# Kernel optimization log

Hardware: AMD Instinct MI355X
Metric: run time of the kernel (lower is better)

Reference implementation:

```python
import jax, jax.numpy as jnp
import numpy as np

V = 32000   # vocab
T = 256     # context len
C = 384     # n_embed
H = 6       # heads
D = 64      # head dim (HEAD_SIZE // NUM_HEADS)
L = 6       # blocks
B = 16      # batch
FF = 4 * C


def setup_inputs() -> dict:
    key = jax.random.key(0)
    ks = jax.random.split(key, 16)
    s = 0.02
    p = {}
    p["x_ids"] = jax.random.randint(ks[0], (B, T), 0, V)
    p["y_ids"] = jax.random.randint(ks[1], (B, T), 0, V)
    p["tok_emb"] = jax.random.normal(ks[2], (V, C), jnp.float32) * s
    p["pos_emb"] = jax.random.normal(ks[3], (T, C), jnp.float32) * s
    p["Wq"] = jax.random.normal(ks[4], (L, H, C, D), jnp.float32) * s
    p["Wk"] = jax.random.normal(ks[5], (L, H, C, D), jnp.float32) * s
    p["Wv"] = jax.random.normal(ks[6], (L, H, C, D), jnp.float32) * s
    p["Wo"] = jax.random.normal(ks[7], (L, H * D, C), jnp.float32) * s
    p["bo"] = jnp.zeros((L, C), jnp.float32)
    p["ln1_s"] = jnp.ones((L, C), jnp.float32)
    p["ln1_b"] = jnp.zeros((L, C), jnp.float32)
    p["ln2_s"] = jnp.ones((L, C), jnp.float32)
    p["ln2_b"] = jnp.zeros((L, C), jnp.float32)
    p["W1"] = jax.random.normal(ks[8], (L, C, FF), jnp.float32) * s
    p["b1"] = jnp.zeros((L, FF), jnp.float32)
    p["W2"] = jax.random.normal(ks[9], (L, FF, C), jnp.float32) * s
    p["b2"] = jnp.zeros((L, C), jnp.float32)
    p["lnf_s"] = jnp.ones((C,), jnp.float32)
    p["lnf_b"] = jnp.zeros((C,), jnp.float32)
    p["Whead"] = jax.random.normal(ks[10], (C, V), jnp.float32) * s
    p["bhead"] = jnp.zeros((V,), jnp.float32)
    return p


def _ln(x, scale, bias, eps=1e-5):
    m = x.mean(-1, keepdims=True)
    v = ((x - m) ** 2).mean(-1, keepdims=True)
    return (x - m) * jax.lax.rsqrt(v + eps) * scale + bias


def reference(x_ids, y_ids, tok_emb, pos_emb, Wq, Wk, Wv, Wo, bo,
              ln1_s, ln1_b, ln2_s, ln2_b, W1, b1, W2, b2,
              lnf_s, lnf_b, Whead, bhead):
    Bq, Tq = x_ids.shape
    x = tok_emb[x_ids] + pos_emb[:Tq]                      # [B,T,C]
    mask = jnp.tril(jnp.ones((Tq, Tq), bool))
    scale = C ** -0.5  # NOTE: original scales by input dim C, not head dim
    for l in range(L):
        h = _ln(x, ln1_s[l], ln1_b[l])
        q = jnp.einsum('btc,hcd->bhtd', h, Wq[l])
        k = jnp.einsum('btc,hcd->bhtd', h, Wk[l])
        v = jnp.einsum('btc,hcd->bhtd', h, Wv[l])
        att = jnp.einsum('bhtd,bhsd->bhts', q, k) * scale
        att = jnp.where(mask, att, -jnp.inf)
        att = jax.nn.softmax(att, axis=-1)
        o = jnp.einsum('bhts,bhsd->bhtd', att, v)
        o = o.transpose(0, 2, 1, 3).reshape(Bq, Tq, H * D)  # concat heads
        x = x + o @ Wo[l] + bo[l]
        h2 = _ln(x, ln2_s[l], ln2_b[l])
        x = x + jax.nn.relu(h2 @ W1[l] + b1[l]) @ W2[l] + b2[l]
    x = _ln(x, lnf_s, lnf_b)
    logits = x @ Whead + bhead                             # [B,T,V]
    logp = jax.nn.log_softmax(logits, axis=-1)
    loss = -jnp.take_along_axis(logp, y_ids[..., None], axis=-1).mean()
    return (logits, loss)
```

## Files before the change

### kernel.cpp

```cpp
#include <hip/hip_runtime.h>

typedef unsigned short u16;
typedef u16   u16x8 __attribute__((ext_vector_type(8)));
typedef short s16x8 __attribute__((ext_vector_type(8)));
typedef float f32x4 __attribute__((ext_vector_type(4)));

#define NV 32000
#define NT 256
#define NC 384
#define NH 6
#define ND 64
#define NL 6
#define NB 16
#define NFF 1536
#define NM (NB*NT)
#define QKVSZ (NB*NH*NT*ND)
#define NSLAB (NV/64)

__device__ __forceinline__ u16 f2bf(float f){
    unsigned x = __builtin_bit_cast(unsigned, f);
    x += 0x7fffu + ((x>>16)&1u);
    return (u16)(x>>16);
}

__device__ __forceinline__ void gload_lds16(const u16* g, u16* l){
    __builtin_amdgcn_global_load_lds((const __attribute__((address_space(1))) unsigned int*)g,
                                     (__attribute__((address_space(3))) unsigned int*)l, 16, 0, 0);
}

template<int N> __device__ __forceinline__ void wait_vm(){
    static_assert(N>=0 && N<=4, "add literal");
    if constexpr (N==0) asm volatile("s_waitcnt vmcnt(0)" ::: "memory");
    if constexpr (N==4) asm volatile("s_waitcnt vmcnt(4)" ::: "memory");
}
__device__ __forceinline__ void bar(){
    asm volatile("" ::: "memory");
    __builtin_amdgcn_s_barrier();
    asm volatile("" ::: "memory");
}

__global__ __launch_bounds__(256) void embed_ln(const int* __restrict__ ids,
        const float* __restrict__ tok, const float* __restrict__ pos,
        const float* __restrict__ sc, const float* __restrict__ bi,
        float* __restrict__ x, u16* __restrict__ out){
    int row  = blockIdx.x*4 + (threadIdx.x>>6);
    int lane = threadIdx.x & 63;
    int t = row & (NT-1);
    const float* tr = tok + (size_t)ids[row]*NC;
    const float* pr = pos + (size_t)t*NC;
    float* xr = x + (size_t)row*NC;
    float v[6]; float sum = 0.f, sq = 0.f;
    #pragma unroll
    for (int i=0;i<6;++i){
        int c = lane+64*i;
        v[i] = tr[c] + pr[c];
        xr[c] = v[i];
        sum += v[i]; sq += v[i]*v[i];
    }
    #pragma unroll
    for (int off=1; off<64; off<<=1){ sum += __shfl_xor(sum,off); sq += __shfl_xor(sq,off); }
    float mean = sum*(1.f/NC);
    float rstd = rsqrtf(sq*(1.f/NC) - mean*mean + 1e-5f);
    u16* orow = out + (size_t)row*NC;
    #pragma unroll
    for (int i=0;i<6;++i){ int c = lane+64*i; orow[c] = f2bf((v[i]-mean)*rstd*sc[c] + bi[c]); }
}

__global__ __launch_bounds__(256) void ln_kernel(const float* __restrict__ x,
        const float* __restrict__ sc, const float* __restrict__ bi, u16* __restrict__ out){
    int row  = blockIdx.x*4 + (threadIdx.x>>6);
    int lane = threadIdx.x & 63;
    const float* xr = x + (size_t)row*NC;
    float v[6]; float sum = 0.f, sq = 0.f;
    #pragma unroll
    for (int i=0;i<6;++i){ v[i]=xr[lane+64*i]; sum+=v[i]; sq+=v[i]*v[i]; }
    #pragma unroll
    for (int off=1; off<64; off<<=1){ sum += __shfl_xor(sum,off); sq += __shfl_xor(sq,off); }
    float mean = sum*(1.f/NC);
    float rstd = rsqrtf(sq*(1.f/NC) - mean*mean + 1e-5f);
    u16* orow = out + (size_t)row*NC;
    #pragma unroll
    for (int i=0;i<6;++i){ int c = lane+64*i; orow[c] = f2bf((v[i]-mean)*rstd*sc[c] + bi[c]); }
}

struct TDesc {
    const float* in; u16* out;
    int Cc; int nx; int perZ; int obDiv; int oStride; int start;
    long inBatch; long oS1; long oS2; float scale;
};
struct TPack { TDesc d[7]; };

__global__ __launch_bounds__(256) void tconv_all(TPack p){
    __shared__ float tile[32][33];
    int bid = blockIdx.x;
    int e = 0;
    #pragma unroll
    for (int i=1;i<7;++i) e += (bid >= p.d[i].start) ? 1 : 0;
    TDesc D = p.d[e];
    int local = bid - D.start;
    int bz  = local / D.perZ; int rem = local - bz*D.perZ;
    int cy  = rem / D.nx;     int cx  = rem - cy*D.nx;
    int r0 = cy*32, c0 = cx*32;
    const float* ib = D.in + (size_t)bz*D.inBatch;
    u16* ob = D.out + (size_t)(bz/D.obDiv)*D.oS1 + (size_t)(bz%D.obDiv)*D.oS2;
    int tx = threadIdx.x & 31, ty = threadIdx.x >> 5;
    #pragma unroll
    for (int i=0;i<4;++i) tile[ty+8*i][tx] = ib[(size_t)(r0+ty+8*i)*D.Cc + (c0+tx)];
    __syncthreads();
    #pragma unroll
    for (int i=0;i<4;++i) ob[(size_t)(c0+ty+8*i)*D.oStride + (r0+tx)] = f2bf(tile[tx][ty+8*i]*D.scale);
}

template<int EPI, int BM, int BN>
__global__ __launch_bounds__(256,4) void gemm_bt(
        const u16* __restrict__ A, const u16* __restrict__ Bt,
        const float* __restrict__ bias, float* __restrict__ resid,
        u16* __restrict__ outb,
        int M, int N, int K){
    constexpr int WM = BM/2, WN = BN/2, MI = WM/16, NI = WN/16;
    __shared__ u16 As[2*BM*32];
    __shared__ u16 Bs[2*BN*32];
    int tid = threadIdx.x;
    int lane = tid & 63, wid = tid >> 6;
    int wm = wid >> 1, wn = wid & 1;
    int l15 = lane & 15, lg = lane >> 4;
    int bx = blockIdx.x, by = blockIdx.y;
    int m0 = by * BM, n0 = bx * BN;
    f32x4 acc[MI][NI];
    #pragma unroll
    for (int a=0;a<MI;++a)
        #pragma unroll
        for (int b=0;b<NI;++b) acc[a][b] = f32x4{0.f,0.f,0.f,0.f};

    int nk = K >> 6;
    for (int kk = 0; kk < nk; ++kk){
        int k0 = kk << 6;
        #pragma unroll
        for (int h=0;h<2;++h){
            if constexpr (BM >= 64){
                #pragma unroll
                for (int i=0;i<BM/64;++i){
                    int o   = i*4096 + tid*16;
                    int row = o >> 6;
                    int kb  = (o & 63) >> 1;
                    gload_lds16(A + (size_t)(m0+row)*K + (k0+h*32+kb), &As[h*BM*32 + (o>>1)]);
                }
            } else {
                if (tid < BM*4){
                    int o = tid*16;
                    int row = o >> 6;
                    int kb  = (o & 63) >> 1;
                    gload_lds16(A + (size_t)(m0+row)*K + (k0+h*32+kb), &As[h*BM*32 + (o>>1)]);
                }
            }
            #pragma unroll
            for (int i=0;i<BN/64;++i){
                int o   = i*4096 + tid*16;
                int row = o >> 6;
                int kb  = (o & 63) >> 1;
                gload_lds16(Bt + (size_t)(n0+row)*K + (k0+h*32+kb), &Bs[h*BN*32 + (o>>1)]);
            }
        }
        asm volatile("s_waitcnt vmcnt(0)" ::: "memory");
        __syncthreads();
        #pragma unroll
        for (int ks=0;ks<2;++ks){
            s16x8 af[MI];
            #pragma unroll
            for (int mi=0;mi<MI;++mi) af[mi] = *(const s16x8*)&As[ks*BM*32 + (wm*WM+mi*16+l15)*32 + lg*8];
            #pragma unroll
            for (int ni=0;ni<NI;++ni){
                s16x8 bfr = *(const s16x8*)&Bs[ks*BN*32 + (wn*WN+ni*16+l15)*32 + lg*8];
                #pragma unroll
                for (int mi=0;mi<MI;++mi)
                    acc[mi][ni] = __builtin_amdgcn_mfma_f32_16x16x32_bf16(af[mi], bfr, acc[mi][ni], 0,0,0);
            }
        }
        __syncthreads();
    }

    #pragma unroll
    for (int mi=0;mi<MI;++mi){
        #pragma unroll
        for (int ni=0;ni<NI;++ni){
            #pragma unroll
            for (int r=0;r<4;++r){
                int mg = m0 + wm*WM + mi*16 + lg*4 + r;
                int ng = n0 + wn*WN + ni*16 + l15;
                float c = acc[mi][ni][r];
                if (EPI == 0){
                    int which = ng / NC; int hd = ng - which*NC;
                    int hh = hd >> 6, d = hd & 63;
                    int bb = mg >> 8, tt = mg & (NT-1);
                    outb[(size_t)which*QKVSZ + ((size_t)(bb*NH+hh)*NT + tt)*ND + d] = f2bf(c);
                } else if (EPI == 1){
                    float* pp = resid + (size_t)mg*N + ng;
                    *pp = *pp + c + bias[ng];
                } else if (EPI == 2){
                    outb[(size_t)mg*N + ng] = f2bf(fmaxf(c + bias[ng], 0.f));
                }
            }
        }
    }
}

__global__ __launch_bounds__(256,4) void gemm_head(
        const u16* __restrict__ A, const u16* __restrict__ Bt,
        const float* __restrict__ bias,
        float* __restrict__ outf, float* __restrict__ lpart,
        int M, int N, int K){
    constexpr int BM=128, BN=128, WM=64, WN=64, MI=4, NI=4;
    __shared__ u16 As[2][BM*32];
    __shared__ u16 Bs[2][BN*32];
    int tid = threadIdx.x;
    int lane = tid & 63, wid = tid >> 6;
    int wm = wid >> 1, wn = wid & 1;
    int l15 = lane & 15, lg = lane >> 4;
    int nwg = gridDim.x*gridDim.y;
    int orig = blockIdx.y*gridDim.x + blockIdx.x;
    int swz = (orig&7)*(nwg>>3) + (orig>>3);
    int by = swz & 31;
    int bx = swz >> 5;
    int m0 = by * BM, n0 = bx * BN;
    f32x4 acc[MI][NI];
    #pragma unroll
    for (int a=0;a<MI;++a)
        #pragma unroll
        for (int b=0;b<NI;++b) acc[a][b] = f32x4{0.f,0.f,0.f,0.f};

    auto STAGE = [&](int kt, int buf){
        int k0 = kt << 5;
        #pragma unroll
        for (int i=0;i<2;++i){
            int o   = i*4096 + tid*16;
            int row = o >> 6;
            int kb  = (o & 63) >> 1;
            gload_lds16(A + (size_t)(m0+row)*K + (k0+kb), &As[buf][o>>1]);
        }
        #pragma unroll
        for (int i=0;i<2;++i){
            int o   = i*4096 + tid*16;
            int row = o >> 6;
            int kb  = (o & 63) >> 1;
            gload_lds16(Bt + (size_t)(n0+row)*K + (k0+kb), &Bs[buf][o>>1]);
        }
    };

    int nk = K >> 5;
    STAGE(0, 0);
    for (int t = 0; t < nk; ++t){
        int buf = t & 1;
        if (t+1 < nk){ STAGE(t+1, buf^1); wait_vm<4>(); }
        else         { wait_vm<0>(); }
        bar();
        s16x8 af[MI];
        #pragma unroll
        for (int mi=0;mi<MI;++mi) af[mi] = *(const s16x8*)&As[buf][(wm*WM+mi*16+l15)*32 + lg*8];
        #pragma unroll
        for (int ni=0;ni<NI;++ni){
            s16x8 bfr = *(const s16x8*)&Bs[buf][(wn*WN+ni*16+l15)*32 + lg*8];
            #pragma unroll
            for (int mi=0;mi<MI;++mi)
                acc[mi][ni] = __builtin_amdgcn_mfma_f32_16x16x32_bf16(af[mi], bfr, acc[mi][ni], 0,0,0);
        }
        bar();
    }

    float es[MI][4];
    #pragma unroll
    for (int mi=0;mi<MI;++mi)
        #pragma unroll
        for (int r=0;r<4;++r) es[mi][r] = 0.f;
    #pragma unroll
    for (int mi=0;mi<MI;++mi)
        #pragma unroll
        for (int ni=0;ni<NI;++ni)
            #pragma unroll
            for (int r=0;r<4;++r){
                int mg = m0 + wm*WM + mi*16 + lg*4 + r;
                int ng = n0 + wn*WN + ni*16 + l15;
                float val = acc[mi][ni][r] + bias[ng];
                outf[(size_t)mg*N + ng] = val;
                es[mi][r] += __expf(val);
            }
    #pragma unroll
    for (int mi=0;mi<MI;++mi)
        #pragma unroll
        for (int r=0;r<4;++r){
            float s = es[mi][r];
            s += __shfl_xor(s,1); s += __shfl_xor(s,2);
            s += __shfl_xor(s,4); s += __shfl_xor(s,8);
            if (l15 == 0){
                int mg = m0 + wm*WM + mi*16 + lg*4 + r;
                lpart[(size_t)mg*NSLAB + bx*2 + wn] = s;
            }
        }
}

__global__ __launch_bounds__(256,2) void attn_kernel(const u16* __restrict__ qkv, u16* __restrict__ o){
    int blk = blockIdx.x;
    int qt = blk & 3, bh = blk >> 2;
    int b = bh / NH, h = bh - b*NH;
    int tid = threadIdx.x, lane = tid & 63, w = tid >> 6;
    int l15 = lane & 15, lg = lane >> 4;
    __shared__ u16 Ks[256*72];
    __shared__ u16 Vt[64*264];
    __shared__ u16 Ps[4][16*72];
    const u16* qb = qkv + (size_t)bh*NT*ND;
    const u16* kb = qb + QKVSZ;
    const u16* vb = kb + QKVSZ;
    int nit = (qt+1)*2;
    for (int it=0; it<nit; ++it){
        int idx = it*256 + tid;
        int e0 = idx*8;
        int row = e0 >> 6, col = e0 & 63;
        *(u16x8*)&Ks[row*72+col] = *(const u16x8*)(kb + e0);
        u16x8 vv = *(const u16x8*)(vb + e0);
        #pragma unroll
        for (int j=0;j<8;++j) Vt[(col+j)*264 + row] = vv[j];
    }
    const u16* qrow = qb + (size_t)(qt*64 + w*16 + l15)*ND;
    s16x8 qf[2];
    qf[0] = *(const s16x8*)(qrow + lg*8);
    qf[1] = *(const s16x8*)(qrow + 32 + lg*8);
    __syncthreads();

    f32x4 oacc[4]; float l_[4];
    #pragma unroll
    for (int c=0;c<4;++c){ oacc[c]=f32x4{0.f,0.f,0.f,0.f}; l_[c]=0.f; }
    u16* Pw = &Ps[w][0];

    for (int kt=0; kt<=qt; ++kt){
        f32x4 sacc[4];
        #pragma unroll
        for (int c=0;c<4;++c) sacc[c]=f32x4{0.f,0.f,0.f,0.f};
        #pragma unroll
        for (int ks=0;ks<2;++ks){
            s16x8 kf[4];
            #pragma unroll
            for (int ni=0;ni<4;++ni)
                kf[ni] = *(const s16x8*)&Ks[(kt*64+ni*16+l15)*72 + ks*32 + lg*8];
            #pragma unroll
            for (int ni=0;ni<4;++ni)
                sacc[ni] = __builtin_amdgcn_mfma_f32_16x16x32_bf16(qf[ks], kf[ni], sacc[ni], 0,0,0);
        }
        if (kt == qt){
            #pragma unroll
            for (int ni=0;ni<4;++ni)
                #pragma unroll
                for (int r=0;r<4;++r)
                    if (ni*16+l15 > w*16+lg*4+r) sacc[ni][r] = -1e30f;
        }
        #pragma unroll
        for (int r=0;r<4;++r){
            float rs = 0.f;
            #pragma unroll
            for (int ni=0;ni<4;++ni){
                float p = __expf(sacc[ni][r]);
                sacc[ni][r] = p;
                rs += p;
                Pw[(lg*4+r)*72 + ni*16 + l15] = f2bf(p);
            }
            rs += __shfl_xor(rs,1); rs += __shfl_xor(rs,2);
            rs += __shfl_xor(rs,4); rs += __shfl_xor(rs,8);
            l_[r] += rs;
        }
        #pragma unroll
        for (int ks=0;ks<2;++ks){
            s16x8 pf, vf[4];
            pf = *(const s16x8*)&Pw[l15*72 + ks*32 + lg*8];
            #pragma unroll
            for (int ni=0;ni<4;++ni)
                vf[ni] = *(const s16x8*)&Vt[(ni*16+l15)*264 + kt*64 + ks*32 + lg*8];
            #pragma unroll
            for (int ni=0;ni<4;++ni)
                oacc[ni] = __builtin_amdgcn_mfma_f32_16x16x32_bf16(pf, vf[ni], oacc[ni], 0,0,0);
        }
    }
    #pragma unroll
    for (int ni=0;ni<4;++ni)
        #pragma unroll
        for (int r=0;r<4;++r){
            int t = qt*64 + w*16 + lg*4 + r;
            int d = ni*16 + l15;
            o[((size_t)(b*NT + t))*NC + h*ND + d] = f2bf(oacc[ni][r] / l_[r]);
        }
}

__global__ __launch_bounds__(256) void loss_rows2(const float* __restrict__ lpart,
        const float* __restrict__ logits, const int* __restrict__ y, float* __restrict__ rowloss){
    int row  = blockIdx.x*4 + (threadIdx.x>>6);
    int lane = threadIdx.x & 63;
    const float* pr = lpart + (size_t)row*NSLAB;
    float s = 0.f;
    for (int i = lane; i < NSLAB; i += 64) s += pr[i];
    #pragma unroll
    for (int off=1; off<64; off<<=1) s += __shfl_xor(s, off);
    if (lane==0)
        rowloss[row] = logf(s) - logits[(size_t)row*NV + y[row]];
}

__global__ __launch_bounds__(256) void loss_final(const float* __restrict__ rowloss, float* __restrict__ out){
    int tid = threadIdx.x;
    float s = 0.f;
    for (int i = tid; i < NM; i += 256) s += rowloss[i];
    #pragma unroll
    for (int off=1; off<64; off<<=1) s += __shfl_xor(s, off);
    __shared__ float ss[4];
    if ((tid&63)==0) ss[tid>>6]=s;
    __syncthreads();
    if (tid==0) out[0] = (ss[0]+ss[1]+ss[2]+ss[3]) * (1.f/NM);
}

extern "C" void kernel_launch(void* const* d_in, const int* in_sizes, int n_in,
                              void* d_out, int out_size, void* d_ws, size_t ws_size,
                              hipStream_t stream){
    const int*   x_ids = (const int*)  d_in[0];
    const int*   y_ids = (const int*)  d_in[1];
    const float* tok   = (const float*)d_in[2];
    const float* pos   = (const float*)d_in[3];
    const float* Wq    = (const float*)d_in[4];
    const float* Wk    = (const float*)d_in[5];
    const float* Wv    = (const float*)d_in[6];
    const float* Wo    = (const float*)d_in[7];
    const float* bo    = (const float*)d_in[8];
    const float* ln1s  = (const float*)d_in[9];
    const float* ln1b  = (const float*)d_in[10];
    const float* ln2s  = (const float*)d_in[11];
    const float* ln2b  = (const float*)d_in[12];
    const float* W1    = (const float*)d_in[13];
    const float* b1    = (const float*)d_in[14];
    const float* W2    = (const float*)d_in[15];
    const float* b2    = (const float*)d_in[16];
    const float* lnfs  = (const float*)d_in[17];
    const float* lnfb  = (const float*)d_in[18];
    const float* Wh    = (const float*)d_in[19];
    const float* bh    = (const float*)d_in[20];

    float* logits = (float*)d_out;
    float* lossp  = logits + (size_t)NM*NV;

    char* ws = (char*)d_ws;
    auto alloc = [&](size_t bytes)->char*{ char* p = ws; ws += (bytes + 255) & ~(size_t)255; return p; };
    float* xf    = (float*)alloc((size_t)NM*NC*4);
    u16*   hbf   = (u16*)  alloc((size_t)NM*NC*2);
    u16*   qkvb  = (u16*)  alloc((size_t)3*QKVSZ*2);
    u16*   obf   = (u16*)  alloc((size_t)NM*NC*2);
    u16*   f1bf  = (u16*)  alloc((size_t)NM*NFF*2);
    u16*   qkvw  = (u16*)  alloc((size_t)NL*1152*NC*2);
    u16*   wot   = (u16*)  alloc((size_t)NL*NC*NC*2);
    u16*   w1t   = (u16*)  alloc((size_t)NL*NFF*NC*2);
    u16*   w2t   = (u16*)  alloc((size_t)NL*NC*NFF*2);
    u16*   wht   = (u16*)  alloc((size_t)NV*NC*2);
    float* part  = (float*)alloc((size_t)NM*4);
    float* lpart = (float*)qkvb;

    const float qscale = 0.051031036307982884f;

    TPack tp;
    tp.d[0] = {Wq, qkvw + 0*(NC*NC), ND,  2,  24, NH, NC, 0,     (long)NC*ND, (long)1152*NC, (long)ND*NC, qscale};
    tp.d[1] = {Wk, qkvw + 1*(NC*NC), ND,  2,  24, NH, NC, 864,   (long)NC*ND, (long)1152*NC, (long)ND*NC, 1.f};
    tp.d[2] = {Wv, qkvw + 2*(NC*NC), ND,  2,  24, NH, NC, 1728,  (long)NC*ND, (long)1152*NC, (long)ND*NC, 1.f};
    tp.d[3] = {Wo, wot,              NC, 12, 144, 1,  NC, 2592,  (long)NC*NC, (long)NC*NC,   0,           1.f};
    tp.d[4] = {W1, w1t,             NFF, 48, 576, 1,  NC, 3456,  (long)NC*NFF,(long)NFF*NC,  0,           1.f};
    tp.d[5] = {W2, w2t,              NC, 12, 576, 1, NFF, 6912,  (long)NFF*NC,(long)NC*NFF,  0,           1.f};
    tp.d[6] = {Wh, wht,              NV,1000,12000,1, NC, 10368, 0,           0,             0,           1.f};
    tconv_all<<<22368,256,0,stream>>>(tp);

    embed_ln<<<NM/4,256,0,stream>>>(x_ids, tok, pos, ln1s, ln1b, xf, hbf);
    for (int l = 0; l < NL; ++l){
        gemm_bt<0,64,128><<<dim3(1152/128, NM/64),256,0,stream>>>(hbf, qkvw + (size_t)l*1152*NC,
                nullptr, nullptr, qkvb, NM, 1152, NC);
        attn_kernel<<<NB*NH*4,256,0,stream>>>(qkvb, obf);
        gemm_bt<1,32,128><<<dim3(NC/128, NM/32),256,0,stream>>>(obf, wot + (size_t)l*NC*NC,
                bo + l*NC, xf, nullptr, NM, NC, NC);
        ln_kernel<<<NM/4,256,0,stream>>>(xf, ln2s + l*NC, ln2b + l*NC, hbf);
        gemm_bt<2,64,128><<<dim3(NFF/128, NM/64),256,0,stream>>>(hbf, w1t + (size_t)l*NFF*NC,
                b1 + l*NFF, nullptr, f1bf, NM, NFF, NC);
        gemm_bt<1,32,128><<<dim3(NC/128, NM/32),256,0,stream>>>(f1bf, w2t + (size_t)l*NC*NFF,
                b2 + l*NC, xf, nullptr, NM, NC, NFF);
        if (l < NL-1)
            ln_kernel<<<NM/4,256,0,stream>>>(xf, ln1s + (l+1)*NC, ln1b + (l+1)*NC, hbf);
        else
            ln_kernel<<<NM/4,256,0,stream>>>(xf, lnfs, lnfb, hbf);
    }
    gemm_head<<<dim3(NV/128, NM/128),256,0,stream>>>(hbf, wht, bh, logits, lpart, NM, NV, NC);
    loss_rows2<<<NM/4,256,0,stream>>>(lpart, logits, y_ids, part);
    loss_final<<<1,256,0,stream>>>(part, lossp);
}
```

Before: 753.5 us.

## Store V pre-transposed from QKV GEMM epilogue to avoid LDS transpose

The QKV projection epilogue now writes the V section in a [b,h,d,t] transposed layout using 4-wide vector stores. The attention kernel then loads V into its transposed shared buffer with 16-byte vector writes, replacing the per-element scattered LDS stores. This removes the costly element-wise transpose into LDS in attention, at the cost of a different global layout for V that both kernels must agree on.

Result: no change. 752.2 us (-0.2%).

```diff
diff --git a/kernel.cpp b/kernel.cpp
--- a/kernel.cpp
+++ b/kernel.cpp
@@ -1,6 +1,7 @@
 #include <hip/hip_runtime.h>
 
 typedef unsigned short u16;
+typedef u16   u16x4 __attribute__((ext_vector_type(4)));
 typedef u16   u16x8 __attribute__((ext_vector_type(8)));
 typedef short s16x8 __attribute__((ext_vector_type(8)));
 typedef float f32x4 __attribute__((ext_vector_type(4)));
@@ -183,21 +184,34 @@
     for (int mi=0;mi<MI;++mi){
         #pragma unroll
         for (int ni=0;ni<NI;++ni){
-            #pragma unroll
-            for (int r=0;r<4;++r){
-                int mg = m0 + wm*WM + mi*16 + lg*4 + r;
+            if (EPI == 0){
                 int ng = n0 + wn*WN + ni*16 + l15;
-                float c = acc[mi][ni][r];
-                if (EPI == 0){
-                    int which = ng / NC; int hd = ng - which*NC;
-                    int hh = hd >> 6, d = hd & 63;
-                    int bb = mg >> 8, tt = mg & (NT-1);
-                    outb[(size_t)which*QKVSZ + ((size_t)(bb*NH+hh)*NT + tt)*ND + d] = f2bf(c);
-                } else if (EPI == 1){
-                    float* pp = resid + (size_t)mg*N + ng;
-                    *pp = *pp + c + bias[ng];
-                } else if (EPI == 2){
-                    outb[(size_t)mg*N + ng] = f2bf(fmaxf(c + bias[ng], 0.f));
+                int which = ng / NC; int hd = ng - which*NC;
+                int hh = hd >> 6, d = hd & 63;
+                int mgb = m0 + wm*WM + mi*16 + lg*4;
+                int bb = mgb >> 8, tt = mgb & (NT-1);
+                if (which == 2){
+                    u16x4 v;
+                    #pragma unroll
+                    for (int r=0;r<4;++r) v[r] = f2bf(acc[mi][ni][r]);
+                    *(u16x4*)(outb + (size_t)2*QKVSZ + ((size_t)(bb*NH+hh)*ND + d)*NT + tt) = v;
+                } else {
+                    #pragma unroll
+                    for (int r=0;r<4;++r)
+                        outb[(size_t)which*QKVSZ + ((size_t)(bb*NH+hh)*NT + tt+r)*ND + d] = f2bf(acc[mi][ni][r]);
+                }
+            } else {
+                #pragma unroll
+                for (int r=0;r<4;++r){
+                    int mg = m0 + wm*WM + mi*16 + lg*4 + r;
+                    int ng = n0 + wn*WN + ni*16 + l15;
+                    float c = acc[mi][ni][r];
+                    if (EPI == 1){
+                        float* pp = resid + (size_t)mg*N + ng;
+                        *pp = *pp + c + bias[ng];
+                    } else if (EPI == 2){
+                        outb[(size_t)mg*N + ng] = f2bf(fmaxf(c + bias[ng], 0.f));
+                    }
                 }
             }
         }
@@ -307,17 +321,21 @@
     __shared__ u16 Vt[64*264];
     __shared__ u16 Ps[4][16*72];
     const u16* qb = qkv + (size_t)bh*NT*ND;
-    const u16* kb = qb + QKVSZ;
-    const u16* vb = kb + QKVSZ;
+    const u16* kb = qkv + QKVSZ + (size_t)bh*NT*ND;
+    const u16* vb = qkv + (size_t)2*QKVSZ + (size_t)bh*ND*NT;
     int nit = (qt+1)*2;
     for (int it=0; it<nit; ++it){
-        int idx = it*256 + tid;
-        int e0 = idx*8;
+        int e0 = (it*256 + tid)*8;
         int row = e0 >> 6, col = e0 & 63;
         *(u16x8*)&Ks[row*72+col] = *(const u16x8*)(kb + e0);
-        u16x8 vv = *(const u16x8*)(vb + e0);
-        #pragma unroll
-        for (int j=0;j<8;++j) Vt[(col+j)*264 + row] = vv[j];
+    }
+    for (int kt2=0; kt2<=qt; ++kt2){
+        #pragma unroll
+        for (int it=0; it<2; ++it){
+            int e0 = (it*256 + tid)*8;
+            int d = e0 >> 6, t = e0 & 63;
+            *(u16x8*)&Vt[d*264 + kt2*64 + t] = *(const u16x8*)(vb + (size_t)d*NT + kt2*64 + t);
+        }
     }
     const u16* qrow = qb + (size_t)(qt*64 + w*16 + l15)*ND;
     s16x8 qf[2];
```
